# Kernel tuning notes

Hardware: AMD Instinct MI355X
Metric: run time of the kernel (lower is better)

The kernel has to match this reference:

```python
import jax, jax.numpy as jnp
import numpy as np

N = 50000      # nodes
E = 800000     # edges (avg degree 16)
C = 32         # channels per degree (deg0 and deg1)
HRAD = 32      # radial MLP hidden
L = 4          # attention layers (plus 1 output layer)
HEADS = 4
EPS = 1e-6
NRAD = 7 * C   # rk00, rk10, rv00, rv10, rv11, rv01, rv11b


def setup_inputs() -> dict:
    key = jax.random.key(0)
    ks = jax.random.split(key, 16)
    L1 = L + 1
    s = 0.1
    return {
        "pos": jax.random.normal(ks[0], (N, 3), jnp.float32),
        "f0": jax.random.normal(ks[1], (N, C), jnp.float32),
        "f1": jax.random.normal(ks[2], (N, C, 3), jnp.float32),
        "src": jax.random.randint(ks[3], (E,), 0, N, jnp.int32),
        "dst": jax.random.randint(ks[4], (E,), 0, N, jnp.int32),
        "W1": jax.random.normal(ks[5], (L1, 1, HRAD), jnp.float32) * s,
        "b1": jnp.zeros((L1, HRAD), jnp.float32),
        "W2": jax.random.normal(ks[6], (L1, HRAD, NRAD), jnp.float32) * s,
        "b2": jnp.zeros((L1, NRAD), jnp.float32),
        "Wq": jax.random.normal(ks[7], (L1, C, C), jnp.float32) * s,
        "Wo0": jax.random.normal(ks[8], (L1, C, C), jnp.float32) * s,
        "Wo1": jax.random.normal(ks[9], (L1, C, C), jnp.float32) * s,
        "Ws0": jax.random.normal(ks[10], (L1, C, C), jnp.float32) * s,
        "Ws1": jax.random.normal(ks[11], (L1, C, C), jnp.float32) * s,
        "bg": jnp.zeros((L, C), jnp.float32),
    }


def _attn_layer(f0, f1, u, rlen, src, dst, n, heads,
                W1, b1, W2, b2, Wq, Wo0, Wo1, Ws0, Ws1):
    # radial network, channel-wise modulation per interaction path
    h = jax.nn.relu(rlen[:, None] @ W1 + b1)            # [E, HRAD]
    R = h @ W2 + b2                                     # [E, 7C]
    rk00, rk10, rv00, rv10, rv11, rv01, rv11b = jnp.split(R, 7, axis=-1)
    f0s = f0[src]                                       # [E, C]
    f1s = f1[src]                                       # [E, C, 3]
    dot1 = jnp.einsum('ecd,ed->ec', f1s, u)             # deg1 -> invariant [E, C]
    # equivariant keys (deg0) and values (deg0 + deg1)
    k0 = rk00 * f0s + rk10 * dot1                       # [E, C]
    v0 = rv00 * f0s + rv10 * dot1                       # [E, C]
    v1 = rv11[..., None] * f1s + (rv01 * f0s + rv11b * dot1)[..., None] * u[:, None, :]  # [E, C, 3]
    # multi-head attention logits on invariants
    ch = C // heads
    q = (f0 @ Wq)[dst].reshape(-1, heads, ch)           # [E, H, ch]
    kh = k0.reshape(-1, heads, ch)
    logits = (q * kh).sum(-1) / np.sqrt(ch)             # [E, H]
    # segment softmax over incoming edges of each dst node
    m = jax.ops.segment_max(logits, dst, num_segments=n)
    e = jnp.exp(logits - m[dst])
    z = jax.ops.segment_sum(e, dst, num_segments=n)
    alpha = e / (z[dst] + EPS)                          # [E, H]
    ac = jnp.repeat(alpha, ch, axis=1)                  # [E, C]
    o0 = jax.ops.segment_sum(ac * v0, dst, num_segments=n)                  # [N, C]
    o1 = jax.ops.segment_sum(ac[..., None] * v1, dst, num_segments=n)       # [N, C, 3]
    # self-interaction + skip
    out0 = o0 @ Wo0 + f0 @ Ws0
    out1 = jnp.einsum('ncd,ce->ned', o1, Wo1) + jnp.einsum('ncd,ce->ned', f1, Ws1)
    return out0, out1


def _forward(pos, f0, f1, src, dst, W1, b1, W2, b2, Wq, Wo0, Wo1, Ws0, Ws1, bg):
    n = f0.shape[0]
    # edge-wise basis (l=0,1 spherical harmonics ~ unit direction) and radial distance
    rel = pos[dst] - pos[src]                           # [E, 3]
    rlen = jnp.linalg.norm(rel, axis=-1)                # [E]
    u = rel / (rlen + EPS)[:, None]                     # [E, 3]
    for i in range(L):
        f0, f1 = _attn_layer(f0, f1, u, rlen, src, dst, n, HEADS,
                             W1[i], b1[i], W2[i], b2[i], Wq[i],
                             Wo0[i], Wo1[i], Ws0[i], Ws1[i])
        # GProjRelu: relu on invariants, norm-gated relu on deg-1
        f0 = jax.nn.relu(f0)
        n1 = jnp.linalg.norm(f1, axis=-1)               # [N, C]
        f1 = f1 * (jax.nn.relu(n1 + bg[i]) / (n1 + EPS))[..., None]
    # final output layer: single head, no nonlinearity
    f0, f1 = _attn_layer(f0, f1, u, rlen, src, dst, n, 1,
                         W1[L], b1[L], W2[L], b2[L], Wq[L],
                         Wo0[L], Wo1[L], Ws0[L], Ws1[L])
    return f0, f1


def reference(pos, f0, f1, src, dst, W1, b1, W2, b2, Wq, Wo0, Wo1, Ws0, Ws1, bg):
    return _forward(pos, f0, f1, src, dst, W1, b1, W2, b2, Wq, Wo0, Wo1, Ws0, Ws1, bg)
```

## Files before the change

### kernel.cpp

```cpp
#include <hip/hip_runtime.h>
#include <math.h>

#define CCH 32
#define NCH 224
#define NIV 33
#define HRAD 32
#define ET 16


__global__ void hist_kernel(const int* __restrict__ dst, int* __restrict__ counts, int E) {
  int e = blockIdx.x * 256 + threadIdx.x;
  if (e < E) atomicAdd(&counts[dst[e]], 1);
}

__global__ void scan1_kernel(const int* __restrict__ counts, int* __restrict__ offs,
                             int* __restrict__ bsums, int n) {
  __shared__ int sd[1024];
  int t = threadIdx.x;
  int i = blockIdx.x * 1024 + t;
  int v = (i < n) ? counts[i] : 0;
  sd[t] = v;
  __syncthreads();
  for (int o = 1; o < 1024; o <<= 1) {
    int add = (t >= o) ? sd[t - o] : 0;
    __syncthreads();
    sd[t] += add;
    __syncthreads();
  }
  if (i < n) offs[i] = sd[t] - v;
  if (t == 1023) bsums[blockIdx.x] = sd[1023];
}

__global__ void scan2_kernel(int* bsums, int nb) {
  if (threadIdx.x == 0 && blockIdx.x == 0) {
    int acc = 0;
    for (int i = 0; i < nb; i++) { int v = bsums[i]; bsums[i] = acc; acc += v; }
  }
}

__global__ void scan3_kernel(int* __restrict__ offs, const int* __restrict__ bsums,
                             int* __restrict__ cursor, int n, int E) {
  int i = blockIdx.x * 256 + threadIdx.x;
  if (i < n) {
    int v = offs[i] + bsums[i >> 10];
    offs[i] = v;
    cursor[i] = v;
  } else if (i == n) {
    offs[n] = E;
  }
}

__global__ void scatter_kernel(const float* __restrict__ pos, const int* __restrict__ src,
                               const int* __restrict__ dst, int* __restrict__ cursor,
                               int* __restrict__ esrcS, float4* __restrict__ egeoS, int E) {
  int e = blockIdx.x * 256 + threadIdx.x;
  if (e >= E) return;
  int s = src[e], d = dst[e];
  float rx = pos[d * 3 + 0] - pos[s * 3 + 0];
  float ry = pos[d * 3 + 1] - pos[s * 3 + 1];
  float rz = pos[d * 3 + 2] - pos[s * 3 + 2];
  float rl = sqrtf(rx * rx + ry * ry + rz * rz);
  float inv = 1.0f / (rl + 1e-6f);
  int p = atomicAdd(&cursor[d], 1);
  esrcS[p] = s;
  egeoS[p] = make_float4(rx * inv, ry * inv, rz * inv, rl);
}


__global__ void pwl_build_kernel(const float* __restrict__ W1, const float* __restrict__ b1,
                                 const float* __restrict__ W2, const float* __restrict__ b2,
                                 float2* __restrict__ coef, float* __restrict__ tks) {
  int l = blockIdx.x / NIV;
  int iv = blockIdx.x - l * NIV;
  int tid = threadIdx.x;
  const float* w1 = W1 + l * HRAD;
  const float* bb1 = b1 + l * HRAD;
  const float* w2 = W2 + l * HRAD * NCH;
  const float* bb2 = b2 + l * NCH;
  __shared__ float a_s[HRAD], b_s[HRAD], t_s[HRAD], t_sorted[HRAD];
  if (tid < HRAD) {
    float a = w1[tid], b = bb1[tid];
    a_s[tid] = a; b_s[tid] = b;
    t_s[tid] = (a != 0.0f) ? (-b / a) : 1e30f;
  }
  __syncthreads();
  if (tid < HRAD) {
    float tj = t_s[tid];
    int rank = 0;
    for (int k = 0; k < HRAD; k++) {
      float tk = t_s[k];
      rank += (tk < tj) || (tk == tj && k < tid);
    }
    t_sorted[rank] = tj;
    if (iv == 0) tks[l * HRAD + tid] = tj;
  }
  __syncthreads();
  if (tid < NCH) {
    int k = tid;
    double lo = (iv == 0) ? (double)t_sorted[0] - 1.0 : (double)t_sorted[iv - 1];
    double hi = (iv == NIV - 1) ? (double)t_sorted[HRAD - 1] + 1.0 : (double)t_sorted[iv];
    double rm = 0.5 * (lo + hi);
    if (iv == 0) rm = (double)t_sorted[0] - 1.0;
    if (iv == NIV - 1) rm = (double)t_sorted[HRAD - 1] + 1.0;
    float alpha = bb2[k];
    float beta = 0.0f;
    for (int j = 0; j < HRAD; j++) {
      if ((double)a_s[j] * rm + (double)b_s[j] > 0.0) {
        float w = w2[j * NCH + k];
        alpha = fmaf(w, b_s[j], alpha);
        beta = fmaf(w, a_s[j], beta);
      }
    }
    coef[l * (NIV * NCH) + iv * NCH + (k & 31) * 7 + (k >> 5)] = make_float2(alpha, beta);
  }
}


__global__ __launch_bounds__(512) void pack_kernel(
    const float* __restrict__ f0, const float* __restrict__ f1,
    const float* __restrict__ Wq0, float scale0,
    float4* __restrict__ fpk, float* __restrict__ qbuf, int n) {
  __shared__ float sWq[1024];
  __shared__ float sF0[ET * 32];
  int tid = threadIdx.x;
  for (int i = tid; i < 1024; i += 512) sWq[i] = Wq0[i];
  __syncthreads();
  int nl = tid >> 5, c = tid & 31;
  for (int base = blockIdx.x * ET; base < n; base += gridDim.x * ET) {
    int node = base + nl;
    float v0 = 0.f, x = 0.f, y = 0.f, z = 0.f;
    if (node < n) {
      v0 = f0[(size_t)node * 32 + c];
      size_t b = ((size_t)node * 32 + c) * 3;
      x = f1[b]; y = f1[b + 1]; z = f1[b + 2];
      fpk[(size_t)node * 32 + c] = make_float4(v0, x, y, z);
    }
    sF0[nl * 32 + c] = v0;
    __syncthreads();
    if (node < n) {
      float q = 0.f;
#pragma unroll
      for (int k = 0; k < 32; k++) q = fmaf(sF0[nl * 32 + k], sWq[k * 32 + c], q);
      qbuf[(size_t)node * 32 + c] = q * scale0;
    }
    __syncthreads();
  }
}


template<int CTRL>
__device__ __forceinline__ float dpp_xor_add(float t) {
  return t + __int_as_float(__builtin_amdgcn_update_dpp(
      0, __float_as_int(t), CTRL, 0xF, 0xF, true));
}

template<int CH>
__global__ __launch_bounds__(1024) void node_kernel(
    const float4* __restrict__ fpk, const float* __restrict__ qbuf,
    float4* __restrict__ Opk,
    const int* __restrict__ esrcS, const float4* __restrict__ egeoS,
    const int* __restrict__ offs,
    const float2* __restrict__ coefG, const float* __restrict__ tkG,
    int n) {
  __shared__ float2 sCoef[NIV * NCH];
  __shared__ float sTk[CCH];
  int tid = threadIdx.x;
  for (int i = tid; i < NIV * NCH; i += 1024) sCoef[i] = coefG[i];
  if (tid < CCH) sTk[tid] = tkG[tid];
  __syncthreads();

  int lane = tid & 63;
  int wid = tid >> 6;
  int c = lane & 31;
  int half = lane >> 5;
  float tk_c = sTk[c];

  int stride = gridDim.x * 16;
  int node = blockIdx.x * 16 + wid;

  int start = 0, end = 0;
  float qs = 0.f;
  int pA = 0;
  float4 pgA = make_float4(0, 0, 0, 0);
  if (node < n) {
    start = offs[node];
    end = offs[node + 1];
    qs = qbuf[(size_t)node * 32 + c];
    int j0 = start + half;
    if (j0 < end) { pA = esrcS[j0]; pgA = egeoS[j0]; }
  }

  for (; node < n; node += stride) {
    int nnode = node + stride;
    int nstart = 0, nend = 0;
    float nqs = 0.f;
    if (nnode < n) {
      nstart = offs[nnode];
      nend = offs[nnode + 1];
      nqs = qbuf[(size_t)nnode * 32 + c];
    }

    float m = -INFINITY, z = 0.0f;
    float o0 = 0.0f, o10 = 0.0f, o11 = 0.0f, o12 = 0.0f;

    int j = start + half;
    int sB = 0;
    float4 gA = pgA, gB = make_float4(0, 0, 0, 0);
    float4 FA = make_float4(0, 0, 0, 0);
    if (j < end) {
      FA = fpk[(size_t)pA * 32 + c];
    }
    if (j + 2 < end) { sB = esrcS[j + 2]; gB = egeoS[j + 2]; }

    unsigned long long msk = __ballot(gA.w > tk_c);
    int iv = half ? (int)__popcll(msk >> 32) : (int)__popcll(msk & 0xFFFFFFFFull);
    const float2* cf = sCoef + (iv * 32 + c) * 7;
    float2 cq0 = cf[0], cq1 = cf[1], cq2 = cf[2], cq3 = cf[3];
    float2 cq4 = cf[4], cq5 = cf[5], cq6 = cf[6];

    while (j < end) {
      float4 g = gA;
      float4 F = FA;
      float2 q0 = cq0, q1 = cq1, q2 = cq2, q3 = cq3;
      float2 q4 = cq4, q5 = cq5, q6 = cq6;
      int j2 = j + 2;
      if (j2 < end) {
        FA = fpk[(size_t)sB * 32 + c];
        gA = gB;
        if (j2 + 2 < end) { sB = esrcS[j2 + 2]; gB = egeoS[j2 + 2]; }
      }
      msk = __ballot(gA.w > tk_c);
      iv = half ? (int)__popcll(msk >> 32) : (int)__popcll(msk & 0xFFFFFFFFull);
      cf = sCoef + (iv * 32 + c) * 7;
      cq0 = cf[0]; cq1 = cf[1]; cq2 = cf[2]; cq3 = cf[3];
      cq4 = cf[4]; cq5 = cf[5]; cq6 = cf[6];

      float r = g.w;
      float rk00 = fmaf(q0.y, r, q0.x), rk10 = fmaf(q1.y, r, q1.x);
      float rv00 = fmaf(q2.y, r, q2.x), rv10 = fmaf(q3.y, r, q3.x);
      float rv11 = fmaf(q4.y, r, q4.x), rv01 = fmaf(q5.y, r, q5.x);
      float rv11b = fmaf(q6.y, r, q6.x);
      float dot1 = fmaf(F.y, g.x, fmaf(F.z, g.y, F.w * g.z));
      float k0 = fmaf(rk00, F.x, rk10 * dot1);
      float t = qs * k0;
      t = dpp_xor_add<0xB1>(t);
      t = dpp_xor_add<0x4E>(t);
      t = dpp_xor_add<0x141>(t);
      if constexpr (CH == 32) {
        t = dpp_xor_add<0x140>(t);
        t = t + __int_as_float(__builtin_amdgcn_ds_swizzle(
                __float_as_int(t), 0x401F));
      }
      float mn = fmaxf(m, t);
      float a = __builtin_amdgcn_exp2f(m - mn);
      float p = __builtin_amdgcn_exp2f(t - mn);
      m = mn;
      z = fmaf(z, a, p);
      float v0 = fmaf(rv00, F.x, rv10 * dot1);
      float sg = fmaf(rv01, F.x, rv11b * dot1);
      o0  = fmaf(o0,  a, p * v0);
      o10 = fmaf(o10, a, p * fmaf(rv11, F.y, sg * g.x));
      o11 = fmaf(o11, a, p * fmaf(rv11, F.z, sg * g.y));
      o12 = fmaf(o12, a, p * fmaf(rv11, F.w, sg * g.z));
      j = j2;
    }

    pA = 0;
    pgA = make_float4(0, 0, 0, 0);
    if (nnode < n) {
      int nj = nstart + half;
      if (nj < nend) { pA = esrcS[nj]; pgA = egeoS[nj]; }
    }

    float mo  = __shfl_xor(m, 32, 64);
    float zo  = __shfl_xor(z, 32, 64);
    float p0  = __shfl_xor(o0, 32, 64);
    float p10 = __shfl_xor(o10, 32, 64);
    float p11 = __shfl_xor(o11, 32, 64);
    float p12 = __shfl_xor(o12, 32, 64);
    float mf = fmaxf(m, mo);
    float aA = 0.0f, aB = 0.0f;
    if (mf > -INFINITY) {
      aA = __builtin_amdgcn_exp2f(m - mf);
      aB = __builtin_amdgcn_exp2f(mo - mf);
    }
    float zf = z * aA + zo * aB;
    float inv = 1.0f / (zf + 1e-6f);
    if (!half) {
      Opk[(size_t)node * 32 + c] = make_float4(
          (o0 * aA + p0 * aB) * inv,
          (o10 * aA + p10 * aB) * inv,
          (o11 * aA + p11 * aB) * inv,
          (o12 * aA + p12 * aB) * inv);
    }

    start = nstart;
    end = nend;
    qs = nqs;
  }
}


__global__ __launch_bounds__(512) void epi_kernel(
    const float4* __restrict__ Opk, float4* __restrict__ fpk,
    const float* __restrict__ Wo0G, const float* __restrict__ Ws0G,
    const float* __restrict__ Wo1G, const float* __restrict__ Ws1G,
    const float* __restrict__ bgG,
    const float* __restrict__ WqN, float* __restrict__ qbuf, float scaleN,
    float* __restrict__ out0, float* __restrict__ out1,
    int mode, int n) {
  __shared__ float4 sW[32 * 32];
  __shared__ float  sWq[32 * 32];
  __shared__ float4 sO[ET * 32];
  __shared__ float4 sF[ET * 32];
  __shared__ float  sF0[ET * 32];
  int tid = threadIdx.x;
  for (int i = tid; i < 1024; i += 512) {
    sW[i] = make_float4(Wo0G[i], Ws0G[i], Wo1G[i], Ws1G[i]);
    if (mode == 0) sWq[i] = WqN[i];
  }
  __syncthreads();
  int nl = tid >> 5;
  int c  = tid & 31;
  for (int base = blockIdx.x * ET; base < n; base += gridDim.x * ET) {
    int node = base + nl;
    bool valid = node < n;
    if (valid) {
      sO[tid] = Opk[(size_t)node * 32 + c];
      sF[tid] = fpk[(size_t)node * 32 + c];
    }
    __syncthreads();
    float a0 = 0.f, ax = 0.f, ay = 0.f, az = 0.f;
#pragma unroll
    for (int k = 0; k < 32; k++) {
      float4 O = sO[nl * 32 + k];
      float4 F = sF[nl * 32 + k];
      float4 w = sW[k * 32 + c];
      a0 = fmaf(O.x, w.x, fmaf(F.x, w.y, a0));
      ax = fmaf(O.y, w.z, fmaf(F.y, w.w, ax));
      ay = fmaf(O.z, w.z, fmaf(F.z, w.w, ay));
      az = fmaf(O.w, w.z, fmaf(F.w, w.w, az));
    }
    if (mode == 0) {
      float f0n = fmaxf(a0, 0.f);
      float n1 = sqrtf(fmaf(ax, ax, fmaf(ay, ay, az * az)));
      float gate = fmaxf(n1 + bgG[c], 0.f) / (n1 + 1e-6f);
      if (valid) fpk[(size_t)node * 32 + c] = make_float4(f0n, ax * gate, ay * gate, az * gate);
      sF0[nl * 32 + c] = f0n;
      __syncthreads();
      if (valid) {
        float q = 0.f;
#pragma unroll
        for (int k = 0; k < 32; k++) q = fmaf(sF0[nl * 32 + k], sWq[k * 32 + c], q);
        qbuf[(size_t)node * 32 + c] = q * scaleN;
      }
      __syncthreads();
    } else {
      if (valid) {
        out0[(size_t)node * 32 + c] = a0;
        size_t b = ((size_t)node * 32 + c) * 3;
        out1[b] = ax; out1[b + 1] = ay; out1[b + 2] = az;
      }
      __syncthreads();
    }
  }
}


extern "C" void kernel_launch(void* const* d_in, const int* in_sizes, int n_in,
                              void* d_out, int out_size, void* d_ws, size_t ws_size,
                              hipStream_t stream) {
  const float* pos = (const float*)d_in[0];
  const float* f0  = (const float*)d_in[1];
  const float* f1  = (const float*)d_in[2];
  const int* src   = (const int*)d_in[3];
  const int* dst   = (const int*)d_in[4];
  const float* W1  = (const float*)d_in[5];
  const float* b1  = (const float*)d_in[6];
  const float* W2  = (const float*)d_in[7];
  const float* b2  = (const float*)d_in[8];
  const float* Wq  = (const float*)d_in[9];
  const float* Wo0 = (const float*)d_in[10];
  const float* Wo1 = (const float*)d_in[11];
  const float* Ws0 = (const float*)d_in[12];
  const float* Ws1 = (const float*)d_in[13];
  const float* bg  = (const float*)d_in[14];

  int N = in_sizes[0] / 3;
  int E = in_sizes[3];

  char* p = (char*)d_ws;
  auto alloc = [&](size_t bytes) {
    char* r = p;
    p += (bytes + 255) & ~(size_t)255;
    return r;
  };
  int* counts   = (int*)alloc((size_t)N * 4);
  int* offs     = (int*)alloc((size_t)(N + 1) * 4);
  int* cursor   = (int*)alloc((size_t)N * 4);
  int* bsums    = (int*)alloc(1024 * 4);
  int* esrcS    = (int*)alloc((size_t)E * 4);
  float4* egeoS = (float4*)alloc((size_t)E * 16);
  float2* coef  = (float2*)alloc((size_t)5 * NIV * NCH * 8);
  float* tks    = (float*)alloc((size_t)5 * HRAD * 4);
  float4* fpk   = (float4*)alloc((size_t)N * CCH * 16);
  float4* Opk   = (float4*)alloc((size_t)N * CCH * 16);
  float* qbuf   = (float*)alloc((size_t)N * CCH * 4);

  pwl_build_kernel<<<5 * NIV, 256, 0, stream>>>(W1, b1, W2, b2, coef, tks);
  hipMemsetAsync(counts, 0, (size_t)N * 4, stream);
  hist_kernel<<<(E + 255) / 256, 256, 0, stream>>>(dst, counts, E);
  int nb = (N + 1023) / 1024;
  scan1_kernel<<<nb, 1024, 0, stream>>>(counts, offs, bsums, N);
  scan2_kernel<<<1, 64, 0, stream>>>(bsums, nb);
  scan3_kernel<<<(N + 1 + 255) / 256, 256, 0, stream>>>(offs, bsums, cursor, N, E);
  scatter_kernel<<<(E + 255) / 256, 256, 0, stream>>>(pos, src, dst, cursor, esrcS, egeoS, E);

  const float LOG2E = 1.4426950408889634f;
  float sc8 = LOG2E / sqrtf(8.0f);
  float sc32 = LOG2E / sqrtf(32.0f);
  int nblk = (N + ET - 1) / ET;
  pack_kernel<<<nblk, 512, 0, stream>>>(f0, f1, Wq, sc8, fpk, qbuf, N);

  float* out0 = (float*)d_out;
  float* out1 = out0 + (size_t)N * CCH;
  for (int l = 0; l < 5; l++) {
    bool last = (l == 4);
    if (last) {
      node_kernel<32><<<512, 1024, 0, stream>>>(
          fpk, qbuf, Opk, esrcS, egeoS, offs,
          coef + (size_t)l * NIV * NCH, tks + l * HRAD, N);
    } else {
      node_kernel<8><<<512, 1024, 0, stream>>>(
          fpk, qbuf, Opk, esrcS, egeoS, offs,
          coef + (size_t)l * NIV * NCH, tks + l * HRAD, N);
    }
    epi_kernel<<<nblk, 512, 0, stream>>>(
        Opk, fpk,
        Wo0 + l * CCH * CCH, Ws0 + l * CCH * CCH,
        Wo1 + l * CCH * CCH, Ws1 + l * CCH * CCH,
        bg + (last ? 0 : l) * CCH,
        Wq + (l + 1 <= 4 ? (l + 1) : 4) * CCH * CCH, qbuf,
        (l + 1 == 4) ? sc32 : sc8,
        out0, out1, last ? 1 : 0, N);
  }
}
```

Measured before the change: 809.5 us.

## Process nodes in descending-degree order to balance per-wave edge loops

Builds a counting-sort permutation of nodes by in-degree, highest first, and has node_kernel walk nodes through this permutation instead of in index order. Each wave then handles nodes of similar degree, which is meant to reduce the wave-level imbalance and tail time caused by variable-length edge loops. The cost is three small extra setup kernels and an extra indirection per node. Output writes now go to scattered node addresses, which loses the contiguity of qbuf and Opk accesses.

```diff
diff --git a/kernel.cpp b/kernel.cpp
--- a/kernel.cpp
+++ b/kernel.cpp
@@ -6,6 +6,7 @@
 #define NIV 33
 #define HRAD 32
 #define ET 16
+#define DBIN 256
 
 
 __global__ void hist_kernel(const int* __restrict__ dst, int* __restrict__ counts, int E) {
@@ -64,6 +65,32 @@
   int p = atomicAdd(&cursor[d], 1);
   esrcS[p] = s;
   egeoS[p] = make_float4(rx * inv, ry * inv, rz * inv, rl);
+}
+
+
+__global__ void deghist_kernel(const int* __restrict__ counts, int* __restrict__ dhist, int n) {
+  int i = blockIdx.x * 256 + threadIdx.x;
+  if (i < n) {
+    int d = counts[i]; if (d > DBIN - 1) d = DBIN - 1;
+    atomicAdd(&dhist[d], 1);
+  }
+}
+
+__global__ void degscan_kernel(int* __restrict__ dhist, int* __restrict__ dcur) {
+  if (threadIdx.x == 0 && blockIdx.x == 0) {
+    int acc = 0;
+    for (int d = DBIN - 1; d >= 0; --d) { dcur[d] = acc; acc += dhist[d]; }
+  }
+}
+
+__global__ void degscatter_kernel(const int* __restrict__ counts, int* __restrict__ dcur,
+                                  int* __restrict__ perm, int n) {
+  int i = blockIdx.x * 256 + threadIdx.x;
+  if (i < n) {
+    int d = counts[i]; if (d > DBIN - 1) d = DBIN - 1;
+    int p = atomicAdd(&dcur[d], 1);
+    perm[p] = i;
+  }
 }
 
 
@@ -159,7 +186,7 @@
     const float4* __restrict__ fpk, const float* __restrict__ qbuf,
     float4* __restrict__ Opk,
     const int* __restrict__ esrcS, const float4* __restrict__ egeoS,
-    const int* __restrict__ offs,
+    const int* __restrict__ offs, const int* __restrict__ perm,
     const float2* __restrict__ coefG, const float* __restrict__ tkG,
     int n) {
   __shared__ float2 sCoef[NIV * NCH];
@@ -176,28 +203,31 @@
   float tk_c = sTk[c];
 
   int stride = gridDim.x * 16;
-  int node = blockIdx.x * 16 + wid;
-
+  int idx = blockIdx.x * 16 + wid;
+
+  int pcur = (idx < n) ? perm[idx] : 0;
+  int pnext = (idx + stride < n) ? perm[idx + stride] : 0;
   int start = 0, end = 0;
   float qs = 0.f;
   int pA = 0;
   float4 pgA = make_float4(0, 0, 0, 0);
-  if (node < n) {
-    start = offs[node];
-    end = offs[node + 1];
-    qs = qbuf[(size_t)node * 32 + c];
+  if (idx < n) {
+    start = offs[pcur];
+    end = offs[pcur + 1];
+    qs = qbuf[pcur * 32 + c];
     int j0 = start + half;
     if (j0 < end) { pA = esrcS[j0]; pgA = egeoS[j0]; }
   }
 
-  for (; node < n; node += stride) {
-    int nnode = node + stride;
+  for (; idx < n; idx += stride) {
+    int nidx = idx + stride;
+    int pnn = (nidx + stride < n) ? perm[nidx + stride] : 0;
     int nstart = 0, nend = 0;
     float nqs = 0.f;
-    if (nnode < n) {
-      nstart = offs[nnode];
-      nend = offs[nnode + 1];
-      nqs = qbuf[(size_t)nnode * 32 + c];
+    if (nidx < n) {
+      nstart = offs[pnext];
+      nend = offs[pnext + 1];
+      nqs = qbuf[pnext * 32 + c];
     }
 
     float m = -INFINITY, z = 0.0f;
@@ -208,7 +238,7 @@
     float4 gA = pgA, gB = make_float4(0, 0, 0, 0);
     float4 FA = make_float4(0, 0, 0, 0);
     if (j < end) {
-      FA = fpk[(size_t)pA * 32 + c];
+      FA = fpk[pA * 32 + c];
     }
     if (j + 2 < end) { sB = esrcS[j + 2]; gB = egeoS[j + 2]; }
 
@@ -225,7 +255,7 @@
       float2 q4 = cq4, q5 = cq5, q6 = cq6;
       int j2 = j + 2;
       if (j2 < end) {
-        FA = fpk[(size_t)sB * 32 + c];
+        FA = fpk[sB * 32 + c];
         gA = gB;
         if (j2 + 2 < end) { sB = esrcS[j2 + 2]; gB = egeoS[j2 + 2]; }
       }
@@ -267,7 +297,7 @@
 
     pA = 0;
     pgA = make_float4(0, 0, 0, 0);
-    if (nnode < n) {
+    if (nidx < n) {
       int nj = nstart + half;
       if (nj < nend) { pA = esrcS[nj]; pgA = egeoS[nj]; }
     }
@@ -287,13 +317,15 @@
     float zf = z * aA + zo * aB;
     float inv = 1.0f / (zf + 1e-6f);
     if (!half) {
-      Opk[(size_t)node * 32 + c] = make_float4(
+      Opk[pcur * 32 + c] = make_float4(
           (o0 * aA + p0 * aB) * inv,
           (o10 * aA + p10 * aB) * inv,
           (o11 * aA + p11 * aB) * inv,
           (o12 * aA + p12 * aB) * inv);
     }
 
+    pcur = pnext;
+    pnext = pnn;
     start = nstart;
     end = nend;
     qs = nqs;
@@ -406,14 +438,21 @@
   float4* fpk   = (float4*)alloc((size_t)N * CCH * 16);
   float4* Opk   = (float4*)alloc((size_t)N * CCH * 16);
   float* qbuf   = (float*)alloc((size_t)N * CCH * 4);
+  int* dhist    = (int*)alloc(DBIN * 4);
+  int* dcur     = (int*)alloc(DBIN * 4);
+  int* perm     = (int*)alloc((size_t)N * 4);
 
   pwl_build_kernel<<<5 * NIV, 256, 0, stream>>>(W1, b1, W2, b2, coef, tks);
   hipMemsetAsync(counts, 0, (size_t)N * 4, stream);
+  hipMemsetAsync(dhist, 0, DBIN * 4, stream);
   hist_kernel<<<(E + 255) / 256, 256, 0, stream>>>(dst, counts, E);
+  deghist_kernel<<<(N + 255) / 256, 256, 0, stream>>>(counts, dhist, N);
   int nb = (N + 1023) / 1024;
   scan1_kernel<<<nb, 1024, 0, stream>>>(counts, offs, bsums, N);
   scan2_kernel<<<1, 64, 0, stream>>>(bsums, nb);
   scan3_kernel<<<(N + 1 + 255) / 256, 256, 0, stream>>>(offs, bsums, cursor, N, E);
+  degscan_kernel<<<1, 64, 0, stream>>>(dhist, dcur);
+  degscatter_kernel<<<(N + 255) / 256, 256, 0, stream>>>(counts, dcur, perm, N);
   scatter_kernel<<<(E + 255) / 256, 256, 0, stream>>>(pos, src, dst, cursor, esrcS, egeoS, E);
 
   const float LOG2E = 1.4426950408889634f;
@@ -428,11 +467,11 @@
     bool last = (l == 4);
     if (last) {
       node_kernel<32><<<512, 1024, 0, stream>>>(
-          fpk, qbuf, Opk, esrcS, egeoS, offs,
+          fpk, qbuf, Opk, esrcS, egeoS, offs, perm,
           coef + (size_t)l * NIV * NCH, tks + l * HRAD, N);
     } else {
       node_kernel<8><<<512, 1024, 0, stream>>>(
-          fpk, qbuf, Opk, esrcS, egeoS, offs,
+          fpk, qbuf, Opk, esrcS, egeoS, offs, perm,
           coef + (size_t)l * NIV * NCH, tks + l * HRAD, N);
     }
     epi_kernel<<<nblk, 512, 0, stream>>>(
```

After: 1.058 ms. 30.7% more time.
